# Kernel optimization log

Measured on AMD Instinct MI355X. Metric: run time of the kernel, lower is better.

The kernel has to match this reference:

```python
import jax, jax.numpy as jnp
import numpy as np

V = 32000   # vocab
H = 512     # hidden = embed dim
L = 2       # lstm layers
S = 64      # source length
K = 3       # beam width
T = 50      # max decode length
BOS = 1


def lstm_cell(x, h, c, Wih, Whh, b):
    # x,h,c: [B,H]; Wih/Whh: [4H,H]; b: [4H]
    z = x @ Wih.T + h @ Whh.T + b
    i, f, g, o = jnp.split(z, 4, axis=-1)
    c = jax.nn.sigmoid(f) * c + jax.nn.sigmoid(i) * jnp.tanh(g)
    h = jax.nn.sigmoid(o) * jnp.tanh(c)
    return h, c


def run_layer(x, Wih, Whh, b):
    # x: [S,B,H] -> outputs [S,B,H], final h,c [B,H]
    B = x.shape[1]
    z = jnp.zeros((B, H), x.dtype)
    def step(carry, xt):
        h, c = carry
        h, c = lstm_cell(xt, h, c, Wih, Whh, b)
        return (h, c), h
    (h, c), ys = jax.lax.scan(step, (z, z), x)
    return ys, h, c


def setup_inputs() -> dict:
    key = jax.random.key(0)
    ks = jax.random.split(key, 10)
    def p(k, shape, s=0.05):
        return jax.random.normal(k, shape, dtype=jnp.float32) * s
    return {
        'input_seq': jax.random.randint(ks[0], (S, 1), 0, V),
        'emb_enc': p(ks[1], (V, H), 0.1),
        'Wih_enc': p(ks[2], (L, 4 * H, H)),
        'Whh_enc': p(ks[3], (L, 4 * H, H)),
        'b_enc': jnp.zeros((L, 4 * H), jnp.float32),
        'emb_dec': p(ks[4], (V, H), 0.1),
        'Wih_dec': p(ks[5], (L, 4 * H, H)),
        'Whh_dec': p(ks[6], (L, 4 * H, H)),
        'b_dec': jnp.zeros((L, 4 * H), jnp.float32),
        'W_c': p(ks[7], (H, 2 * H)),
        'W_out': p(ks[8], (V, H)),
        'b_out': jnp.zeros((V,), jnp.float32),
        'input_length': S,
        'max_length': T,
        'bos': BOS,
    }


def reference(input_seq, emb_enc, Wih_enc, Whh_enc, b_enc,
              emb_dec, Wih_dec, Whh_dec, b_dec, W_c, W_out, b_out,
              input_length, max_length, bos):
    # ---- encoder ----
    x = emb_enc[input_seq[:, 0]][:, None, :]        # [S,1,H]
    hs, cs = [], []
    for l in range(L):
        x, hl, cl = run_layer(x, Wih_enc[l], Whh_enc[l], b_enc[l])
        hs.append(hl); cs.append(cl)
    enc_out = x[:, 0, :]                            # [S,H]
    h = jnp.stack(hs)                               # [L,1,H]
    c = jnp.stack(cs)

    # ---- decoder single step (vectorized over beam) ----
    def decode_step(tokens, h, c):
        x = emb_dec[tokens]                         # [B,H]
        nh, nc = [], []
        for l in range(L):
            hl, cl = lstm_cell(x, h[l], c[l], Wih_dec[l], Whh_dec[l], b_dec[l])
            nh.append(hl); nc.append(cl); x = hl
        attn = jax.nn.softmax(jnp.einsum('sh,bh->bs', enc_out, x), axis=-1)
        ctx = attn @ enc_out                        # [B,H]
        feat = jnp.tanh(jnp.concatenate([x, ctx], -1) @ W_c.T)
        probs = jax.nn.softmax(feat @ W_out.T + b_out)  # [B,V]
        return probs, jnp.stack(nh), jnp.stack(nc)

    # ---- first step (beam expand) ----
    probs, h, c = decode_step(jnp.array([bos]), h, c)
    topv, topi = jax.lax.top_k(probs[0], K)
    scores = jnp.log(topv)                          # [K]
    tokens = topi                                   # [K]
    h = jnp.repeat(h, K, axis=1)                    # [L,K,H]
    c = jnp.repeat(c, K, axis=1)
    backtrack = jnp.full((K, max_length), bos, dtype=jnp.int32)

    # ---- beam search loop ----
    def body(carry, t):
        tokens, h, c, scores, bt = carry
        probs, hn, cn = decode_step(tokens, h, c)   # [K,V]
        topv, topi = jax.lax.top_k(probs, K)        # [K,K]
        cum = jnp.log(topv) + scores[:, None]
        cand_scores, flat = jax.lax.top_k(cum.reshape(-1), K)
        best = topi.reshape(-1)[flat]
        orig = flat // K                            # beam origins
        bt = bt[orig].at[:, t + 1].set(tokens[orig])
        return (best, hn[:, orig, :], cn[:, orig, :], cand_scores, bt), None

    (tokens, h, c, scores, backtrack), _ = jax.lax.scan(
        body, (tokens, h, c, scores, backtrack), jnp.arange(max_length - 1))
    return backtrack[jnp.argmax(scores)]            # [max_length] tokens
```

## Files before the change

kernel.cpp:

```cpp
#include <hip/hip_runtime.h>
#include <math.h>

#define HSZ   512
#define H4    2048
#define SEQ   64
#define VOC   32000
#define BEAM  3
#define TMAX  50

#define LOFF  ((size_t)H4 * HSZ)

__device__ __forceinline__ float wsum(float v) {
#pragma unroll
  for (int off = 32; off; off >>= 1) v += __shfl_xor(v, off, 64);
  return v;
}
__device__ __forceinline__ float dot4(float4 a, float4 b) {
  return a.x * b.x + a.y * b.y + a.z * b.z + a.w * b.w;
}
__device__ __forceinline__ float sigf(float x) { return 1.f / (1.f + expf(-x)); }

__device__ __forceinline__ bool better(float v1, int i1, float v2, int i2) {
  return (v1 > v2) || (v1 == v2 && i1 < i2);
}
__device__ __forceinline__ void ins3(float* v, int* idx, float nv, int ni) {
  if (better(nv, ni, v[2], idx[2])) {
    if (better(nv, ni, v[1], idx[1])) {
      v[2] = v[1]; idx[2] = idx[1];
      if (better(nv, ni, v[0], idx[0])) { v[1] = v[0]; idx[1] = idx[0]; v[0] = nv; idx[0] = ni; }
      else { v[1] = nv; idx[1] = ni; }
    } else { v[2] = nv; idx[2] = ni; }
  }
}


__global__ void __launch_bounds__(512) k_xw1(const float* __restrict__ Wih,
                                             const float* __restrict__ bias,
                                             const float* __restrict__ emb,
                                             const int* __restrict__ seq,
                                             float* __restrict__ xp1) {
  int t    = threadIdx.x & 63;
  int wave = threadIdx.x >> 6;
  int r    = blockIdx.x * 8 + wave;
  int tok  = seq[t];
  const float* xr = emb + (size_t)tok * HSZ;
  const float* wr = Wih + (size_t)r * HSZ;
  float acc = 0.f;
  for (int e = 0; e < HSZ; e += 4) {
    float4 wv = *(const float4*)(wr + e);
    float4 xv = *(const float4*)(xr + e);
    acc += dot4(wv, xv);
  }
  xp1[t * H4 + r] = acc + bias[r];
}

__global__ void __launch_bounds__(512) k_encslot(const float* __restrict__ Whh1,
                                                 const float* __restrict__ Wih2,
                                                 const float* __restrict__ Whh2,
                                                 const float* __restrict__ b2,
                                                 const float* __restrict__ xp1,
                                                 float* __restrict__ h1a, float* __restrict__ c1a,
                                                 float* __restrict__ h2a, float* __restrict__ c2a,
                                                 int s) {
  __shared__ float rowX[HSZ], rowH[HSZ], zl[16];
  int tid = threadIdx.x, wave = tid >> 6, lane = tid & 63;
  bool l2 = blockIdx.x >= 128;
  int t = l2 ? s - 1 : s;
  if (t < 0 || t >= SEQ) return;
  int bb = blockIdx.x & 127;
  int lr = wave >> 1;
  int j  = bb * 4 + lr;
  int g0 = (wave & 1) * 2;
  if (!l2) {
    rowX[tid] = (t > 0) ? h1a[t * HSZ + tid] : 0.f;
    __syncthreads();
    float4 h0 = ((const float4*)rowX)[lane], h1v = ((const float4*)rowX)[lane + 64];
#pragma unroll
    for (int gg = 0; gg < 2; ++gg) {
      int g = g0 + gg;
      int row = j + (g << 9);
      const float4* wr = (const float4*)(Whh1 + (size_t)row * HSZ);
      float zs = wsum(dot4(wr[lane], h0) + dot4(wr[lane + 64], h1v));
      if (lane == 0) zl[lr * 4 + g] = zs + xp1[t * H4 + row];
    }
    __syncthreads();
    if (tid < 4) {
      int j2 = bb * 4 + tid;
      float z0 = zl[tid * 4 + 0], z1 = zl[tid * 4 + 1], z2 = zl[tid * 4 + 2], z3 = zl[tid * 4 + 3];
      float cp = (t > 0) ? c1a[t * HSZ + j2] : 0.f;
      float c = sigf(z1) * cp + sigf(z0) * tanhf(z2);
      c1a[(t + 1) * HSZ + j2] = c;
      h1a[(t + 1) * HSZ + j2] = sigf(z3) * tanhf(c);
    }
  } else {
    rowX[tid] = h1a[(t + 1) * HSZ + tid];
    rowH[tid] = (t > 0) ? h2a[t * HSZ + tid] : 0.f;
    __syncthreads();
    float4 x0 = ((const float4*)rowX)[lane], x1 = ((const float4*)rowX)[lane + 64];
    float4 h0 = ((const float4*)rowH)[lane], h1v = ((const float4*)rowH)[lane + 64];
#pragma unroll
    for (int gg = 0; gg < 2; ++gg) {
      int g = g0 + gg;
      int row = j + (g << 9);
      const float4* wi = (const float4*)(Wih2 + (size_t)row * HSZ);
      const float4* wh = (const float4*)(Whh2 + (size_t)row * HSZ);
      float zs = wsum(dot4(wi[lane], x0) + dot4(wi[lane + 64], x1) +
                      dot4(wh[lane], h0) + dot4(wh[lane + 64], h1v));
      if (lane == 0) zl[lr * 4 + g] = zs + b2[row];
    }
    __syncthreads();
    if (tid < 4) {
      int j2 = bb * 4 + tid;
      float z0 = zl[tid * 4 + 0], z1 = zl[tid * 4 + 1], z2 = zl[tid * 4 + 2], z3 = zl[tid * 4 + 3];
      float cp = (t > 0) ? c2a[t * HSZ + j2] : 0.f;
      float c = sigf(z1) * cp + sigf(z0) * tanhf(z2);
      c2a[(t + 1) * HSZ + j2] = c;
      h2a[(t + 1) * HSZ + j2] = sigf(z3) * tanhf(c);
    }
  }
}


template <int B, int BIN, int MODE>
__global__ void __launch_bounds__(512) k_dcell1(
    const float* __restrict__ Wih, const float* __restrict__ Whh,
    const float* __restrict__ bias,
    const float* __restrict__ emb_dec, const int* __restrict__ bosp,
    const float* __restrict__ h1prev, const float* __restrict__ c1prev,
    const float* __restrict__ h2prev, const float* __restrict__ c2prev,
    const float* __restrict__ pm, const float* __restrict__ ps,
    const float* __restrict__ pv, const int* __restrict__ pi,
    float* __restrict__ hout, float* __restrict__ cout,
    float* __restrict__ hd2p, float* __restrict__ cd2p,
    const float* __restrict__ scores_rd, float* __restrict__ scores_wr,
    const int* __restrict__ tokens_rd, int* __restrict__ tokens_wr,
    int* __restrict__ bt, int ti) {
  __shared__ float xl[B * HSZ], hl[B * HSZ], cl[B * HSZ], zl[8 * B];
  __shared__ float sM[3], sS[3], sV[3][3], sScore[3];
  __shared__ int sI[3][3], sOrig[3], sTokNew[3], sTokOld[3];
  int tid = threadIdx.x, wave = tid >> 6, lane = tid & 63;

  if (MODE >= 1) {
    if (wave < BIN) {
      int b = wave;
      float lm4[4], ls4[4];
      float M = -INFINITY;
#pragma unroll
      for (int q = 0; q < 4; ++q) {
        int blk2 = lane + q * 64;
        lm4[q] = pm[blk2 * 3 + b]; ls4[q] = ps[blk2 * 3 + b];
        M = fmaxf(M, lm4[q]);
      }
#pragma unroll
      for (int off = 32; off; off >>= 1) M = fmaxf(M, __shfl_xor(M, off, 64));
      float S = 0.f;
#pragma unroll
      for (int q = 0; q < 4; ++q) S += ls4[q] * expf(lm4[q] - M);
      S = wsum(S);
      float bv[3] = {-INFINITY, -INFINITY, -INFINITY};
      int bi3[3]  = {0x7fffffff, 0x7fffffff, 0x7fffffff};
#pragma unroll
      for (int q = 0; q < 4; ++q) {
        int blk2 = lane + q * 64;
#pragma unroll
        for (int k = 0; k < 3; ++k)
          ins3(bv, bi3, pv[(blk2 * 3 + b) * 3 + k], pi[(blk2 * 3 + b) * 3 + k]);
      }
#pragma unroll
      for (int off = 32; off; off >>= 1) {
        float ov[3]; int oi[3];
#pragma unroll
        for (int k = 0; k < 3; ++k) { ov[k] = __shfl_xor(bv[k], off, 64); oi[k] = __shfl_xor(bi3[k], off, 64); }
#pragma unroll
        for (int k = 0; k < 3; ++k) ins3(bv, bi3, ov[k], oi[k]);
      }
      if (lane == 0) {
        sM[b] = M; sS[b] = S;
#pragma unroll
        for (int k = 0; k < 3; ++k) { sV[b][k] = bv[k]; sI[b][k] = bi3[k]; }
      }
    }
    __syncthreads();
    if (tid == 0) {
      if (MODE == 1) {
        float off0 = -sM[0] - logf(sS[0]);
        for (int k = 0; k < 3; ++k) {
          sScore[k] = sV[0][k] + off0;
          sTokNew[k] = sI[0][k]; sOrig[k] = 0; sTokOld[k] = 0;
        }
      } else {
        float osc[3];
        for (int b = 0; b < 3; ++b) { osc[b] = scores_rd[b]; sTokOld[b] = tokens_rd[b]; }
        float cum[9];
        for (int b = 0; b < 3; ++b) {
          float o = osc[b] - sM[b] - logf(sS[b]);
          for (int k = 0; k < 3; ++k) cum[b * 3 + k] = sV[b][k] + o;
        }
        bool used[9] = {false, false, false, false, false, false, false, false, false};
        for (int k = 0; k < 3; ++k) {
          int bf = 0; float bb = -INFINITY;
          for (int f = 0; f < 9; ++f)
            if (!used[f] && cum[f] > bb) { bb = cum[f]; bf = f; }
          used[bf] = true;
          sScore[k] = bb;
          int ob = bf / 3;
          sOrig[k] = ob;
          sTokNew[k] = sI[ob][bf - ob * 3];
        }
      }
    }
    __syncthreads();
  }

  if (MODE == 0) {
    int bos = bosp[0];
    for (int i = tid; i < B * HSZ; i += 512) {
      xl[i] = emb_dec[(size_t)bos * HSZ + i];
      hl[i] = h1prev[i]; cl[i] = c1prev[i];
    }
    if (blockIdx.x == 0) {
      for (int i = tid; i < B * HSZ; i += 512) { hd2p[i] = h2prev[i]; cd2p[i] = c2prev[i]; }
    }
  } else {
    for (int i = tid; i < B * HSZ; i += 512) {
      int b = i >> 9, e = i & 511;
      xl[i] = emb_dec[(size_t)sTokNew[b] * HSZ + e];
      hl[i] = h1prev[sOrig[b] * HSZ + e];
      cl[i] = c1prev[sOrig[b] * HSZ + e];
    }
    if (blockIdx.x == 0) {
      for (int i = tid; i < B * HSZ; i += 512) {
        int b = i >> 9, e = i & 511;
        hd2p[i] = h2prev[sOrig[b] * HSZ + e];
        cd2p[i] = c2prev[sOrig[b] * HSZ + e];
      }
      if (MODE == 1) {
        int bos = bosp[0];
        for (int idx = tid; idx < BEAM * TMAX; idx += 512) bt[idx] = bos;
      } else {
        const int* src = bt + (ti & 1) * (BEAM * TMAX);
        int* dst = bt + ((ti + 1) & 1) * (BEAM * TMAX);
        for (int idx = tid; idx < BEAM * TMAX; idx += 512) {
          int k = idx / TMAX, jj = idx % TMAX, o = sOrig[k];
          dst[idx] = (jj == ti + 1) ? sTokOld[o] : src[o * TMAX + jj];
        }
      }
      if (tid < 3) { scores_wr[tid] = sScore[tid]; tokens_wr[tid] = sTokNew[tid]; }
    }
  }
  __syncthreads();

  int lr = wave >> 2;
  int g  = wave & 3;
  int j  = blockIdx.x * 2 + lr;
  int row = j + (g << 9);
  const float4* wi = (const float4*)(Wih + (size_t)row * HSZ);
  const float4* wh = (const float4*)(Whh + (size_t)row * HSZ);
  float4 wi0 = wi[lane], wi1 = wi[lane + 64], wh0 = wh[lane], wh1 = wh[lane + 64];
  float bb = bias[row];
#pragma unroll
  for (int b = 0; b < B; ++b) {
    float4 xv0 = ((const float4*)(xl + b * HSZ))[lane];
    float4 xv1 = ((const float4*)(xl + b * HSZ))[lane + 64];
    float4 hv0 = ((const float4*)(hl + b * HSZ))[lane];
    float4 hv1 = ((const float4*)(hl + b * HSZ))[lane + 64];
    float acc = dot4(wi0, xv0) + dot4(wi1, xv1) + dot4(wh0, hv0) + dot4(wh1, hv1);
    float z = wsum(acc) + bb;
    if (lane == 0) zl[(lr * 4 + g) * B + b] = z;
  }
  __syncthreads();
  for (int q = tid; q < 2 * B; q += 512) {
    int lr2 = q / B, b = q % B;
    int j2 = blockIdx.x * 2 + lr2;
    float z0 = zl[(lr2 * 4 + 0) * B + b], z1 = zl[(lr2 * 4 + 1) * B + b];
    float z2 = zl[(lr2 * 4 + 2) * B + b], z3 = zl[(lr2 * 4 + 3) * B + b];
    float c = sigf(z1) * cl[b * HSZ + j2] + sigf(z0) * tanhf(z2);
    cout[b * HSZ + j2] = c;
    hout[b * HSZ + j2] = sigf(z3) * tanhf(c);
  }
}

template <int B>
__global__ void __launch_bounds__(512) k_dcell2(const float* __restrict__ Wih,
                                                const float* __restrict__ Whh,
                                                const float* __restrict__ bias,
                                                const float* __restrict__ x,
                                                const float* __restrict__ hin,
                                                const float* __restrict__ cin,
                                                float* __restrict__ hout, float* __restrict__ cout) {
  __shared__ float xl[B * HSZ], hl[B * HSZ], cl[B * HSZ], zl[8 * B];
  int tid = threadIdx.x;
  for (int i = tid; i < B * HSZ; i += 512) { xl[i] = x[i]; hl[i] = hin[i]; cl[i] = cin[i]; }
  __syncthreads();
  int wave = tid >> 6, lane = tid & 63;
  int lr = wave >> 2;
  int g  = wave & 3;
  int j  = blockIdx.x * 2 + lr;
  int row = j + (g << 9);
  const float4* wi = (const float4*)(Wih + (size_t)row * HSZ);
  const float4* wh = (const float4*)(Whh + (size_t)row * HSZ);
  float4 wi0 = wi[lane], wi1 = wi[lane + 64], wh0 = wh[lane], wh1 = wh[lane + 64];
  float bb = bias[row];
#pragma unroll
  for (int b = 0; b < B; ++b) {
    float4 xv0 = ((const float4*)(xl + b * HSZ))[lane];
    float4 xv1 = ((const float4*)(xl + b * HSZ))[lane + 64];
    float4 hv0 = ((const float4*)(hl + b * HSZ))[lane];
    float4 hv1 = ((const float4*)(hl + b * HSZ))[lane + 64];
    float acc = dot4(wi0, xv0) + dot4(wi1, xv1) + dot4(wh0, hv0) + dot4(wh1, hv1);
    float z = wsum(acc) + bb;
    if (lane == 0) zl[(lr * 4 + g) * B + b] = z;
  }
  __syncthreads();
  for (int q = tid; q < 2 * B; q += 512) {
    int lr2 = q / B, b = q % B;
    int j2 = blockIdx.x * 2 + lr2;
    float z0 = zl[(lr2 * 4 + 0) * B + b], z1 = zl[(lr2 * 4 + 1) * B + b];
    float z2 = zl[(lr2 * 4 + 2) * B + b], z3 = zl[(lr2 * 4 + 3) * B + b];
    float c = sigf(z1) * cl[b * HSZ + j2] + sigf(z0) * tanhf(z2);
    cout[b * HSZ + j2] = c;
    hout[b * HSZ + j2] = sigf(z3) * tanhf(c);
  }
}

template <int B>
__global__ void __launch_bounds__(512) k_attfeat(const float* __restrict__ h2,
                                                 const float* __restrict__ enc,
                                                 const float* __restrict__ Wc,
                                                 float* __restrict__ feat) {
  __shared__ float xs[BEAM * HSZ], at[BEAM * SEQ], xcs[BEAM * 1024];
  int tid = threadIdx.x;
  for (int i = tid; i < B * HSZ; i += 512) xs[i] = h2[i];
  __syncthreads();
  if (tid < B * SEQ) {
    int b = tid >> 6, s2 = tid & 63;
    const float* er = enc + (s2 + 1) * HSZ;
    const float* xb = xs + b * HSZ;
    float acc = 0.f;
    for (int e = 0; e < HSZ; e += 4) {
      float4 ev = *(const float4*)(er + e);
      acc += ev.x * xb[e] + ev.y * xb[e + 1] + ev.z * xb[e + 2] + ev.w * xb[e + 3];
    }
    at[tid] = acc;
  }
  __syncthreads();
  if (tid < B) {
    float m = -INFINITY;
    for (int s2 = 0; s2 < SEQ; ++s2) m = fmaxf(m, at[tid * SEQ + s2]);
    float s = 0.f;
    for (int s2 = 0; s2 < SEQ; ++s2) { float e = expf(at[tid * SEQ + s2] - m); at[tid * SEQ + s2] = e; s += e; }
    float inv = 1.f / s;
    for (int s2 = 0; s2 < SEQ; ++s2) at[tid * SEQ + s2] *= inv;
  }
  __syncthreads();
  if (tid < 128) {
    int h4 = tid * 4;
    float4 acc[B];
#pragma unroll
    for (int b = 0; b < B; ++b) acc[b] = make_float4(0.f, 0.f, 0.f, 0.f);
    for (int s2 = 0; s2 < SEQ; ++s2) {
      float4 ev = *(const float4*)(enc + (s2 + 1) * HSZ + h4);
#pragma unroll
      for (int b = 0; b < B; ++b) {
        float a = at[b * SEQ + s2];
        acc[b].x += a * ev.x; acc[b].y += a * ev.y; acc[b].z += a * ev.z; acc[b].w += a * ev.w;
      }
    }
#pragma unroll
    for (int b = 0; b < B; ++b) *(float4*)(xcs + b * 1024 + 512 + h4) = acc[b];
  }
  for (int i = tid; i < B * HSZ; i += 512) {
    int b = i >> 9, hcol = i & 511;
    xcs[b * 1024 + hcol] = xs[b * HSZ + hcol];
  }
  __syncthreads();
  int wave = tid >> 6, lane = tid & 63;
  int j = blockIdx.x * 8 + wave;
  const float4* w = (const float4*)(Wc + (size_t)j * 1024);
  float4 w0 = w[lane], w1 = w[lane + 64], w2 = w[lane + 128], w3 = w[lane + 192];
#pragma unroll
  for (int b = 0; b < B; ++b) {
    const float4* xb = (const float4*)(xcs + b * 1024);
    float acc = dot4(w0, xb[lane]) + dot4(w1, xb[lane + 64]) +
                dot4(w2, xb[lane + 128]) + dot4(w3, xb[lane + 192]);
    acc = wsum(acc);
    if (lane == 0) feat[b * HSZ + j] = tanhf(acc);
  }
}

template <int B>
__global__ void __launch_bounds__(512) k_logits(const float* __restrict__ Wout,
                                                const float* __restrict__ bout,
                                                const float* __restrict__ feat,
                                                float* __restrict__ pm, float* __restrict__ ps,
                                                float* __restrict__ pv, int* __restrict__ pi) {
  __shared__ float fst[BEAM * HSZ];
  int tid = threadIdx.x;
  for (int i = tid; i < B * HSZ; i += 512) fst[i] = feat[i];
  __syncthreads();
  int wave = tid >> 6, lane = tid & 63;
  int gid  = blockIdx.x * 8 + wave;
  float4 f0[B], f1[B];
#pragma unroll
  for (int b = 0; b < B; ++b) {
    f0[b] = ((const float4*)(fst + b * HSZ))[lane];
    f1[b] = ((const float4*)(fst + b * HSZ))[lane + 64];
  }
  float m[B], ss[B], tv[B][3];
  int tix[B][3];
#pragma unroll
  for (int b = 0; b < B; ++b) {
    m[b] = -INFINITY; ss[b] = 0.f;
#pragma unroll
    for (int k = 0; k < 3; ++k) { tv[b][k] = -INFINITY; tix[b][k] = 0x7fffffff; }
  }
  for (int k0 = 0; k0 < 16; k0 += 8) {
    float4 a0[8], a1[8]; float ab[8]; int vr[8];
#pragma unroll
    for (int u = 0; u < 8; ++u) {
      int v = gid + (k0 + u) * 2048;
      vr[u] = v;
      if (v < VOC) {
        const float4* wr = (const float4*)(Wout + (size_t)v * HSZ);
        a0[u] = wr[lane]; a1[u] = wr[lane + 64]; ab[u] = bout[v];
      } else {
        a0[u] = make_float4(0.f, 0.f, 0.f, 0.f); a1[u] = a0[u]; ab[u] = 0.f;
      }
    }
#pragma unroll
    for (int u = 0; u < 8; ++u) {
      if (vr[u] >= VOC) continue;
#pragma unroll
      for (int b = 0; b < B; ++b) {
        float acc = wsum(dot4(a0[u], f0[b]) + dot4(a1[u], f1[b])) + ab[u];
        float mo = m[b], mn = fmaxf(mo, acc);
        ss[b] = ss[b] * expf(mo - mn) + expf(acc - mn);
        m[b]  = mn;
        ins3(tv[b], tix[b], acc, vr[u]);
      }
    }
  }
  __shared__ float lm[8][3], lss[8][3], lv[8][3][3];
  __shared__ int li[8][3][3];
  if (lane == 0) {
#pragma unroll
    for (int b = 0; b < B; ++b) {
      lm[wave][b] = m[b]; lss[wave][b] = ss[b];
#pragma unroll
      for (int k = 0; k < 3; ++k) { lv[wave][b][k] = tv[b][k]; li[wave][b][k] = tix[b][k]; }
    }
  }
  __syncthreads();
  if (tid < B) {
    int b = tid;
    float M = -INFINITY;
#pragma unroll
    for (int w2 = 0; w2 < 8; ++w2) M = fmaxf(M, lm[w2][b]);
    float S = 0.f;
#pragma unroll
    for (int w2 = 0; w2 < 8; ++w2) S += lss[w2][b] * expf(lm[w2][b] - M);
    float bv[3] = {-INFINITY, -INFINITY, -INFINITY};
    int bi3[3]  = {0x7fffffff, 0x7fffffff, 0x7fffffff};
#pragma unroll
    for (int w2 = 0; w2 < 8; ++w2)
#pragma unroll
      for (int k = 0; k < 3; ++k) ins3(bv, bi3, lv[w2][b][k], li[w2][b][k]);
    int o = blockIdx.x * 3 + b;
    pm[o] = M; ps[o] = S;
#pragma unroll
    for (int k = 0; k < 3; ++k) { pv[o * 3 + k] = bv[k]; pi[o * 3 + k] = bi3[k]; }
  }
}

__global__ void __launch_bounds__(256) k_tail(const float* __restrict__ pm,
                                              const float* __restrict__ ps,
                                              const float* __restrict__ pv,
                                              const int* __restrict__ pi,
                                              const float* __restrict__ scores_rd,
                                              const int* __restrict__ tokens_rd,
                                              int* __restrict__ bt, int* __restrict__ outp) {
  const int ti = TMAX - 2;
  __shared__ float sM[3], sS[3], sV[3][3], sScore[3];
  __shared__ int sI[3][3], sOrig[3], sTokOld[3], sKstar;
  int tid = threadIdx.x, wave = tid >> 6, lane = tid & 63;
  if (wave < 3) {
    int b = wave;
    float lm4[4], ls4[4];
    float M = -INFINITY;
#pragma unroll
    for (int q = 0; q < 4; ++q) {
      int blk2 = lane + q * 64;
      lm4[q] = pm[blk2 * 3 + b]; ls4[q] = ps[blk2 * 3 + b];
      M = fmaxf(M, lm4[q]);
    }
#pragma unroll
    for (int off = 32; off; off >>= 1) M = fmaxf(M, __shfl_xor(M, off, 64));
    float S = 0.f;
#pragma unroll
    for (int q = 0; q < 4; ++q) S += ls4[q] * expf(lm4[q] - M);
    S = wsum(S);
    float bv[3] = {-INFINITY, -INFINITY, -INFINITY};
    int bi3[3]  = {0x7fffffff, 0x7fffffff, 0x7fffffff};
#pragma unroll
    for (int q = 0; q < 4; ++q) {
      int blk2 = lane + q * 64;
#pragma unroll
      for (int k = 0; k < 3; ++k)
        ins3(bv, bi3, pv[(blk2 * 3 + b) * 3 + k], pi[(blk2 * 3 + b) * 3 + k]);
    }
#pragma unroll
    for (int off = 32; off; off >>= 1) {
      float ov[3]; int oi[3];
#pragma unroll
      for (int k = 0; k < 3; ++k) { ov[k] = __shfl_xor(bv[k], off, 64); oi[k] = __shfl_xor(bi3[k], off, 64); }
#pragma unroll
      for (int k = 0; k < 3; ++k) ins3(bv, bi3, ov[k], oi[k]);
    }
    if (lane == 0) {
      sM[b] = M; sS[b] = S;
#pragma unroll
      for (int k = 0; k < 3; ++k) { sV[b][k] = bv[k]; sI[b][k] = bi3[k]; }
    }
  }
  __syncthreads();
  if (tid == 0) {
    float osc[3];
    for (int b = 0; b < 3; ++b) { osc[b] = scores_rd[b]; sTokOld[b] = tokens_rd[b]; }
    float cum[9];
    for (int b = 0; b < 3; ++b) {
      float o = osc[b] - sM[b] - logf(sS[b]);
      for (int k = 0; k < 3; ++k) cum[b * 3 + k] = sV[b][k] + o;
    }
    bool used[9] = {false, false, false, false, false, false, false, false, false};
    for (int k = 0; k < 3; ++k) {
      int bf = 0; float bb = -INFINITY;
      for (int f = 0; f < 9; ++f)
        if (!used[f] && cum[f] > bb) { bb = cum[f]; bf = f; }
      used[bf] = true;
      sScore[k] = bb;
      sOrig[k] = bf / 3;
    }
    float bb = -INFINITY; int kk = 0;
    for (int k = 0; k < 3; ++k) if (sScore[k] > bb) { bb = sScore[k]; kk = k; }
    sKstar = kk;
  }
  __syncthreads();
  const int* src = bt + (ti & 1) * (BEAM * TMAX);
  int* dst = bt + ((ti + 1) & 1) * (BEAM * TMAX);
  for (int idx = tid; idx < BEAM * TMAX; idx += 256) {
    int k = idx / TMAX, jj = idx % TMAX, o = sOrig[k];
    dst[idx] = (jj == ti + 1) ? sTokOld[o] : src[o * TMAX + jj];
  }
  __syncthreads();
  for (int jj = tid; jj < TMAX; jj += 256) outp[jj] = dst[sKstar * TMAX + jj];
}

extern "C" void kernel_launch(void* const* d_in, const int* in_sizes, int n_in,
                              void* d_out, int out_size, void* d_ws, size_t ws_size,
                              hipStream_t stream) {
  const int*   seq     = (const int*)d_in[0];
  const float* emb_enc = (const float*)d_in[1];
  const float* Wih_enc = (const float*)d_in[2];
  const float* Whh_enc = (const float*)d_in[3];
  const float* b_enc   = (const float*)d_in[4];
  const float* emb_dec = (const float*)d_in[5];
  const float* Wih_dec = (const float*)d_in[6];
  const float* Whh_dec = (const float*)d_in[7];
  const float* b_dec   = (const float*)d_in[8];
  const float* W_c     = (const float*)d_in[9];
  const float* W_out   = (const float*)d_in[10];
  const float* b_out   = (const float*)d_in[11];
  const int*   bosp    = (const int*)d_in[14];

  float* w = (float*)d_ws;
  float* xp1     = w; w += SEQ * H4;
  float* h1a     = w; w += (SEQ + 1) * HSZ;
  float* c1a     = w; w += (SEQ + 1) * HSZ;
  float* h2a     = w; w += (SEQ + 1) * HSZ;
  float* c2a     = w; w += (SEQ + 1) * HSZ;
  float* hdn1    = w; w += 2 * BEAM * HSZ;
  float* cdn1    = w; w += 2 * BEAM * HSZ;
  float* hdn2    = w; w += 2 * BEAM * HSZ;
  float* cdn2    = w; w += 2 * BEAM * HSZ;
  float* hd2p    = w; w += BEAM * HSZ;
  float* cd2p    = w; w += BEAM * HSZ;
  float* feat    = w; w += BEAM * HSZ;
  float* pm      = w; w += 256 * 3;
  float* ps      = w; w += 256 * 3;
  float* pv      = w; w += 256 * 3 * 3;
  float* sb      = w; w += 2 * 4;
  int* pi     = (int*)w; w += 256 * 3 * 3;
  int* tb     = (int*)w; w += 2 * 4;
  int* bt     = (int*)w; w += 2 * BEAM * TMAX + 4;
  int* outp   = (int*)d_out;

  k_xw1<<<256, 512, 0, stream>>>(Wih_enc, b_enc, emb_enc, seq, xp1);
  for (int s = 0; s <= SEQ; ++s)
    k_encslot<<<256, 512, 0, stream>>>(Whh_enc, Wih_enc + LOFF, Whh_enc + LOFF, b_enc + H4,
                                       xp1, h1a, c1a, h2a, c2a, s);

  for (int s = 0; s < TMAX; ++s) {
    int rp = (s - 1) & 1, wp = s & 1;
    if (s == 0) {
      k_dcell1<1, 1, 0><<<256, 512, 0, stream>>>(
          Wih_dec, Whh_dec, b_dec, emb_dec, bosp,
          h1a + SEQ * HSZ, c1a + SEQ * HSZ, h2a + SEQ * HSZ, c2a + SEQ * HSZ,
          pm, ps, pv, pi,
          hdn1 + 0, cdn1 + 0, hd2p, cd2p,
          sb, sb, tb, tb, bt, 0);
      k_dcell2<1><<<256, 512, 0, stream>>>(Wih_dec + LOFF, Whh_dec + LOFF, b_dec + H4,
                                           hdn1 + 0, hd2p, cd2p, hdn2 + 0, cdn2 + 0);
      k_attfeat<1><<<64, 512, 0, stream>>>(hdn2 + 0, h2a, W_c, feat);
      k_logits<1><<<256, 512, 0, stream>>>(W_out, b_out, feat, pm, ps, pv, pi);
    } else {
      float* h1p = hdn1 + rp * BEAM * HSZ; float* c1p = cdn1 + rp * BEAM * HSZ;
      float* h2p = hdn2 + rp * BEAM * HSZ; float* c2p = cdn2 + rp * BEAM * HSZ;
      float* h1o = hdn1 + wp * BEAM * HSZ; float* c1o = cdn1 + wp * BEAM * HSZ;
      float* h2o = hdn2 + wp * BEAM * HSZ; float* c2o = cdn2 + wp * BEAM * HSZ;
      if (s == 1)
        k_dcell1<3, 1, 1><<<256, 512, 0, stream>>>(
            Wih_dec, Whh_dec, b_dec, emb_dec, bosp,
            h1p, c1p, h2p, c2p, pm, ps, pv, pi,
            h1o, c1o, hd2p, cd2p,
            sb + rp * 4, sb + wp * 4, tb + rp * 4, tb + wp * 4, bt, -1);
      else
        k_dcell1<3, 3, 2><<<256, 512, 0, stream>>>(
            Wih_dec, Whh_dec, b_dec, emb_dec, bosp,
            h1p, c1p, h2p, c2p, pm, ps, pv, pi,
            h1o, c1o, hd2p, cd2p,
            sb + rp * 4, sb + wp * 4, tb + rp * 4, tb + wp * 4, bt, s - 2);
      k_dcell2<3><<<256, 512, 0, stream>>>(Wih_dec + LOFF, Whh_dec + LOFF, b_dec + H4,
                                           h1o, hd2p, cd2p, h2o, c2o);
      k_attfeat<3><<<64, 512, 0, stream>>>(h2o, h2a, W_c, feat);
      k_logits<3><<<256, 512, 0, stream>>>(W_out, b_out, feat, pm, ps, pv, pi);
    }
  }
  k_tail<<<1, 256, 0, stream>>>(pm, ps, pv, pi, sb + 4, tb + 4, bt, outp);
}
```

Baseline: 3.595 ms.

## Fuse attention-feature and logits kernels using inter-block flag synchronization

Merges the attention/feature kernel and the logits kernel into one launch of 256 blocks. The first 64 blocks compute the feature vector and publish it with agent-scope atomic stores plus a per-block epoch flag. All blocks spin on those flags before loading feat and running the vocabulary projection. This removes one kernel launch and its gap per decode step, but it relies on the 64 producer blocks being resident alongside the spinning blocks, and it adds spin-wait cost plus a memset.

```diff
diff --git a/kernel.cpp b/kernel.cpp
--- a/kernel.cpp
+++ b/kernel.cpp
@@ -7,6 +7,7 @@
 #define VOC   32000
 #define BEAM  3
 #define TMAX  50
+#define FLS   16
 
 #define LOFF  ((size_t)H4 * HSZ)
 
@@ -31,6 +32,19 @@
       else { v[1] = nv; idx[1] = ni; }
     } else { v[2] = nv; idx[2] = ni; }
   }
+}
+
+__device__ __forceinline__ float agld(const float* p) {
+  return __hip_atomic_load(p, __ATOMIC_RELAXED, __HIP_MEMORY_SCOPE_AGENT);
+}
+__device__ __forceinline__ void agst(float* p, float v) {
+  __hip_atomic_store(p, v, __ATOMIC_RELAXED, __HIP_MEMORY_SCOPE_AGENT);
+}
+__device__ __forceinline__ int agldi(const int* p) {
+  return __hip_atomic_load(p, __ATOMIC_RELAXED, __HIP_MEMORY_SCOPE_AGENT);
+}
+__device__ __forceinline__ void agsti(int* p, int v) {
+  __hip_atomic_store(p, v, __ATOMIC_RELAXED, __HIP_MEMORY_SCOPE_AGENT);
 }
 
 
@@ -324,82 +338,89 @@
 }
 
 template <int B>
-__global__ void __launch_bounds__(512) k_attfeat(const float* __restrict__ h2,
-                                                 const float* __restrict__ enc,
-                                                 const float* __restrict__ Wc,
-                                                 float* __restrict__ feat) {
+__global__ void __launch_bounds__(512) k_atlg(const float* __restrict__ h2,
+                                              const float* __restrict__ enc,
+                                              const float* __restrict__ Wc,
+                                              const float* __restrict__ Wout,
+                                              const float* __restrict__ bout,
+                                              float* __restrict__ feat,
+                                              float* __restrict__ pm, float* __restrict__ ps,
+                                              float* __restrict__ pv, int* __restrict__ pi,
+                                              int* __restrict__ flags, int ep) {
   __shared__ float xs[BEAM * HSZ], at[BEAM * SEQ], xcs[BEAM * 1024];
-  int tid = threadIdx.x;
-  for (int i = tid; i < B * HSZ; i += 512) xs[i] = h2[i];
-  __syncthreads();
-  if (tid < B * SEQ) {
-    int b = tid >> 6, s2 = tid & 63;
-    const float* er = enc + (s2 + 1) * HSZ;
-    const float* xb = xs + b * HSZ;
-    float acc = 0.f;
-    for (int e = 0; e < HSZ; e += 4) {
-      float4 ev = *(const float4*)(er + e);
-      acc += ev.x * xb[e] + ev.y * xb[e + 1] + ev.z * xb[e + 2] + ev.w * xb[e + 3];
-    }
-    at[tid] = acc;
-  }
-  __syncthreads();
-  if (tid < B) {
-    float m = -INFINITY;
-    for (int s2 = 0; s2 < SEQ; ++s2) m = fmaxf(m, at[tid * SEQ + s2]);
-    float s = 0.f;
-    for (int s2 = 0; s2 < SEQ; ++s2) { float e = expf(at[tid * SEQ + s2] - m); at[tid * SEQ + s2] = e; s += e; }
-    float inv = 1.f / s;
-    for (int s2 = 0; s2 < SEQ; ++s2) at[tid * SEQ + s2] *= inv;
-  }
-  __syncthreads();
-  if (tid < 128) {
-    int h4 = tid * 4;
-    float4 acc[B];
-#pragma unroll
-    for (int b = 0; b < B; ++b) acc[b] = make_float4(0.f, 0.f, 0.f, 0.f);
-    for (int s2 = 0; s2 < SEQ; ++s2) {
-      float4 ev = *(const float4*)(enc + (s2 + 1) * HSZ + h4);
-#pragma unroll
-      for (int b = 0; b < B; ++b) {
-        float a = at[b * SEQ + s2];
-        acc[b].x += a * ev.x; acc[b].y += a * ev.y; acc[b].z += a * ev.z; acc[b].w += a * ev.w;
-      }
-    }
-#pragma unroll
-    for (int b = 0; b < B; ++b) *(float4*)(xcs + b * 1024 + 512 + h4) = acc[b];
-  }
-  for (int i = tid; i < B * HSZ; i += 512) {
-    int b = i >> 9, hcol = i & 511;
-    xcs[b * 1024 + hcol] = xs[b * HSZ + hcol];
-  }
-  __syncthreads();
-  int wave = tid >> 6, lane = tid & 63;
-  int j = blockIdx.x * 8 + wave;
-  const float4* w = (const float4*)(Wc + (size_t)j * 1024);
-  float4 w0 = w[lane], w1 = w[lane + 64], w2 = w[lane + 128], w3 = w[lane + 192];
-#pragma unroll
-  for (int b = 0; b < B; ++b) {
-    const float4* xb = (const float4*)(xcs + b * 1024);
-    float acc = dot4(w0, xb[lane]) + dot4(w1, xb[lane + 64]) +
-                dot4(w2, xb[lane + 128]) + dot4(w3, xb[lane + 192]);
-    acc = wsum(acc);
-    if (lane == 0) feat[b * HSZ + j] = tanhf(acc);
-  }
-}
-
-template <int B>
-__global__ void __launch_bounds__(512) k_logits(const float* __restrict__ Wout,
-                                                const float* __restrict__ bout,
-                                                const float* __restrict__ feat,
-                                                float* __restrict__ pm, float* __restrict__ ps,
-                                                float* __restrict__ pv, int* __restrict__ pi) {
   __shared__ float fst[BEAM * HSZ];
-  int tid = threadIdx.x;
-  for (int i = tid; i < B * HSZ; i += 512) fst[i] = feat[i];
-  __syncthreads();
-  int wave = tid >> 6, lane = tid & 63;
-  int gid  = blockIdx.x * 8 + wave;
+  int tid = threadIdx.x, wave = tid >> 6, lane = tid & 63;
+
+  if (blockIdx.x < 64) {
+    for (int i = tid; i < B * HSZ; i += 512) xs[i] = h2[i];
+    __syncthreads();
+    if (tid < B * SEQ) {
+      int b = tid >> 6, s2 = tid & 63;
+      const float* er = enc + (s2 + 1) * HSZ;
+      const float* xb = xs + b * HSZ;
+      float acc = 0.f;
+      for (int e = 0; e < HSZ; e += 4) {
+        float4 ev = *(const float4*)(er + e);
+        acc += ev.x * xb[e] + ev.y * xb[e + 1] + ev.z * xb[e + 2] + ev.w * xb[e + 3];
+      }
+      at[tid] = acc;
+    }
+    __syncthreads();
+    if (tid < B) {
+      float m = -INFINITY;
+      for (int s2 = 0; s2 < SEQ; ++s2) m = fmaxf(m, at[tid * SEQ + s2]);
+      float s = 0.f;
+      for (int s2 = 0; s2 < SEQ; ++s2) { float e = expf(at[tid * SEQ + s2] - m); at[tid * SEQ + s2] = e; s += e; }
+      float inv = 1.f / s;
+      for (int s2 = 0; s2 < SEQ; ++s2) at[tid * SEQ + s2] *= inv;
+    }
+    __syncthreads();
+    if (tid < 128) {
+      int h4 = tid * 4;
+      float4 acc[B];
+#pragma unroll
+      for (int b = 0; b < B; ++b) acc[b] = make_float4(0.f, 0.f, 0.f, 0.f);
+      for (int s2 = 0; s2 < SEQ; ++s2) {
+        float4 ev = *(const float4*)(enc + (s2 + 1) * HSZ + h4);
+#pragma unroll
+        for (int b = 0; b < B; ++b) {
+          float a = at[b * SEQ + s2];
+          acc[b].x += a * ev.x; acc[b].y += a * ev.y; acc[b].z += a * ev.z; acc[b].w += a * ev.w;
+        }
+      }
+#pragma unroll
+      for (int b = 0; b < B; ++b) *(float4*)(xcs + b * 1024 + 512 + h4) = acc[b];
+    }
+    for (int i = tid; i < B * HSZ; i += 512) {
+      int b = i >> 9, hcol = i & 511;
+      xcs[b * 1024 + hcol] = xs[b * HSZ + hcol];
+    }
+    __syncthreads();
+    int j = blockIdx.x * 8 + wave;
+    const float4* w = (const float4*)(Wc + (size_t)j * 1024);
+    float4 w0 = w[lane], w1 = w[lane + 64], w2 = w[lane + 128], w3 = w[lane + 192];
+#pragma unroll
+    for (int b = 0; b < B; ++b) {
+      const float4* xb = (const float4*)(xcs + b * 1024);
+      float acc = dot4(w0, xb[lane]) + dot4(w1, xb[lane + 64]) +
+                  dot4(w2, xb[lane + 128]) + dot4(w3, xb[lane + 192]);
+      acc = wsum(acc);
+      if (lane == 0) agst(&feat[b * HSZ + j], tanhf(acc));
+    }
+    __syncthreads();
+    if (tid == 0) agsti(&flags[blockIdx.x * FLS], ep);
+  }
+
+  if (tid < 64) {
+    long it = 0;
+    while (agldi(&flags[tid * FLS]) < ep && it < 200000000L) ++it;
+  }
+  asm volatile("" ::: "memory");
+  __syncthreads();
+
+  for (int i = tid; i < B * HSZ; i += 512) fst[i] = agld(&feat[i]);
+  __syncthreads();
+  int gid = blockIdx.x * 8 + wave;
   float4 f0[B], f1[B];
 #pragma unroll
   for (int b = 0; b < B; ++b) {
@@ -572,7 +593,8 @@
   const float* b_out   = (const float*)d_in[11];
   const int*   bosp    = (const int*)d_in[14];
 
-  float* w = (float*)d_ws;
+  int* flags = (int*)d_ws;
+  float* w = (float*)d_ws + 64 * FLS;
   float* xp1     = w; w += SEQ * H4;
   float* h1a     = w; w += (SEQ + 1) * HSZ;
   float* c1a     = w; w += (SEQ + 1) * HSZ;
@@ -594,6 +616,8 @@
   int* bt     = (int*)w; w += 2 * BEAM * TMAX + 4;
   int* outp   = (int*)d_out;
 
+  hipMemsetAsync(flags, 0, 64 * FLS * sizeof(int), stream);
+
   k_xw1<<<256, 512, 0, stream>>>(Wih_enc, b_enc, emb_enc, seq, xp1);
   for (int s = 0; s <= SEQ; ++s)
     k_encslot<<<256, 512, 0, stream>>>(Whh_enc, Wih_enc + LOFF, Whh_enc + LOFF, b_enc + H4,
@@ -610,8 +634,8 @@
           sb, sb, tb, tb, bt, 0);
       k_dcell2<1><<<256, 512, 0, stream>>>(Wih_dec + LOFF, Whh_dec + LOFF, b_dec + H4,
                                            hdn1 + 0, hd2p, cd2p, hdn2 + 0, cdn2 + 0);
-      k_attfeat<1><<<64, 512, 0, stream>>>(hdn2 + 0, h2a, W_c, feat);
-      k_logits<1><<<256, 512, 0, stream>>>(W_out, b_out, feat, pm, ps, pv, pi);
+      k_atlg<1><<<256, 512, 0, stream>>>(hdn2 + 0, h2a, W_c, W_out, b_out, feat,
+                                         pm, ps, pv, pi, flags, s + 1);
     } else {
       float* h1p = hdn1 + rp * BEAM * HSZ; float* c1p = cdn1 + rp * BEAM * HSZ;
       float* h2p = hdn2 + rp * BEAM * HSZ; float* c2p = cdn2 + rp * BEAM * HSZ;
@@ -631,8 +655,8 @@
             sb + rp * 4, sb + wp * 4, tb + rp * 4, tb + wp * 4, bt, s - 2);
       k_dcell2<3><<<256, 512, 0, stream>>>(Wih_dec + LOFF, Whh_dec + LOFF, b_dec + H4,
                                            h1o, hd2p, cd2p, h2o, c2o);
-      k_attfeat<3><<<64, 512, 0, stream>>>(h2o, h2a, W_c, feat);
-      k_logits<3><<<256, 512, 0, stream>>>(W_out, b_out, feat, pm, ps, pv, pi);
+      k_atlg<3><<<256, 512, 0, stream>>>(h2o, h2a, W_c, W_out, b_out, feat,
+                                         pm, ps, pv, pi, flags, s + 1);
     }
   }
   k_tail<<<1, 256, 0, stream>>>(pm, ps, pv, pi, sb + 4, tb + 4, bt, outp);
```

After: 3.558 ms (median of 2 runs). Within noise of the previous version (-1.0%).
